# Performance work log

Measured on AMD Instinct MI355X. Metric: run time of the kernel, lower is better.

## Reference

```python
import jax, jax.numpy as jnp
import numpy as np

B, N, M, DIN, HID, L, NC, NH = 8, 1024, 8, 1024, 256, 2, 7, 4
DH = HID // NH
ALPHA = 0.1          # LeakyReLU slope in RGATLayer
NEG = -9e15          # masked-softmax fill value from the source


def setup_inputs() -> dict:
    key = jax.random.key(0)
    ks = jax.random.split(key, 40)
    f32 = jnp.float32
    rn = lambda k, s, sc: jax.random.normal(k, s, f32) * sc
    w = HID ** -0.5
    inp = {
        'x': rn(ks[0], (B, N, DIN), 1.0),
        'adj': jax.random.randint(ks[1], (B, N, N), 0, 2, jnp.int32),
        's_mask': jax.random.randint(ks[2], (B, N, N), 0, 2, jnp.int32),
        's_feature': rn(ks[3], (B, M, DIN), 1.0),
        's_adj': jax.random.uniform(ks[4], (B, M, N), f32),
        'speaker_id': jax.random.randint(ks[5], (B, N), 0, M, jnp.int32),
        'fc1_w': rn(ks[6], (DIN, HID), DIN ** -0.5), 'fc1_b': jnp.zeros((HID,), f32),
        'fc2_w': rn(ks[7], (DIN, HID), DIN ** -0.5), 'fc2_b': jnp.zeros((HID,), f32),
        'gat_W': rn(ks[8], (L, HID, HID), w),
        'gat_a': rn(ks[9], (L, 3 * HID), (3 * HID) ** -0.5),
        'rel_emb': rn(ks[10], (L, 2, HID), 0.1),
        'gru_wz': rn(ks[11], (L, HID, HID), 0.1), 'gru_uz': rn(ks[12], (L, HID, HID), 0.1),
        'gru_wr': rn(ks[13], (L, HID, HID), 0.1), 'gru_ur': rn(ks[14], (L, HID, HID), 0.1),
        'gru_w': rn(ks[15], (L, HID, HID), 0.1), 'gru_u': rn(ks[16], (L, HID, HID), 0.1),
        'mha_wv': rn(ks[17], (L, HID, HID), w), 'mha_bv': jnp.zeros((L, HID), f32),
        'mha_wk': rn(ks[18], (L, HID, HID), w), 'mha_bk': jnp.zeros((L, HID), f32),
        'mha_wq': rn(ks[19], (L, HID, HID), w), 'mha_bq': jnp.zeros((L, HID), f32),
        'mha_wo': rn(ks[20], (L, HID, HID), w), 'mha_bo': jnp.zeros((L, HID), f32),
        'ln_g': jnp.ones((L, HID), f32), 'ln_b': jnp.zeros((L, HID), f32),
        'out_w': rn(ks[21], (HID, NC), w), 'out_b': jnp.zeros((NC,), f32),
    }
    return inp


def _layer_norm(x, g, b):
    mu = jnp.mean(x, -1, keepdims=True)
    var = jnp.mean((x - mu) ** 2, -1, keepdims=True)
    return (x - mu) * jax.lax.rsqrt(var + 1e-5) * g + b


def reference(x, adj, s_mask, s_feature, s_adj, speaker_id,
              fc1_w, fc1_b, fc2_w, fc2_b,
              gat_W, gat_a, rel_emb,
              gru_wz, gru_uz, gru_wr, gru_ur, gru_w, gru_u,
              mha_wv, mha_bv, mha_wk, mha_bk, mha_wq, mha_bq, mha_wo, mha_bo,
              ln_g, ln_b, out_w, out_b):
    # eval mode: dropout is identity. init_way == 'global', att_agg == True.
    H = jax.nn.relu(x @ fc1_w + fc1_b)           # [B,N,HID]
    P = jax.nn.relu(s_feature @ fc2_w + fc2_b)   # [B,M,HID]
    adj_mask = adj > 0
    for l in range(L):
        P_l_1 = jnp.einsum('bmn,bmd->bnd', s_adj, P)  # s_adj^T @ P -> [B,N,HID]
        # ---- RGAT layer (decomposed: never materializes [B,N,N,3*HID]) ----
        h = H @ gat_W[l]                               # [B,N,HID]
        a1, a2, a3 = jnp.split(gat_a[l], 3)
        rel_sc = rel_emb[l] @ a3                       # (2,) per-relation score
        e = jax.nn.leaky_relu((h @ a1)[:, :, None] + (h @ a2)[:, None, :]
                              + jnp.take(rel_sc, s_mask), ALPHA)  # [B,N,N]
        att = jax.nn.softmax(jnp.where(adj_mask, e, jnp.float32(NEG)), axis=2)
        Agg = jax.nn.elu(att @ h)                      # [B,N,HID]
        # ---- Multi-head attention aggregation (replicates source's reshape) ----
        V = (H @ mha_wv[l] + mha_bv[l]).reshape(B * NH, -1, DH)
        Km = (P_l_1 @ mha_wk[l] + mha_bk[l]).reshape(B * NH, -1, DH)
        Qm = (Agg @ mha_wq[l] + mha_bq[l]).reshape(B * NH, -1, DH)
        att2 = jax.nn.softmax(jnp.einsum('bqd,bkd->bqk', Qm, Km) * DH ** -0.5, axis=-1)
        ctx = (att2 @ V).reshape(B, -1, HID)
        H_new = _layer_norm(ctx @ mha_wo[l] + mha_bo[l] + H, ln_g[l], ln_b[l])
        # ---- GRU3d speaker-state update (uses H[l], i.e. pre-update H) ----
        P_agg = jnp.einsum('bmn,bnd->bmd', s_adj, H)   # [B,M,HID]
        z = jax.nn.sigmoid(P @ gru_wz[l] + P_agg @ gru_uz[l])
        r = jax.nn.sigmoid(P @ gru_wr[l] + P_agg @ gru_ur[l])
        h_hat = jnp.tanh(P @ gru_w[l] + r * (P_agg @ gru_u[l]))
        P = (1 - z) * P + z * h_hat
        H = H_new
    # sim_loss
    ps = jnp.einsum('bmd,bkd->bmk', P, P)
    ps = ps * (1.0 - jnp.eye(M, dtype=ps.dtype))
    p_sim = jnp.mean(jnp.mean(jnp.mean(ps, -1), -1), -1)
    logits = H @ out_w + out_b
    return (logits, p_sim)
```

## Files before the change

### kernel.cpp

```cpp
#include <hip/hip_runtime.h>
#include <cmath>

#define B 8
#define N 1024
#define MSP 8
#define DIN 1024
#define HID 256
#define NLAYER 2
#define NCLS 7
#define NHEAD 4
#define DHD 64
#define G (B*NHEAD)
#define SEQ 1024
#define LALPHA 0.1f
#define NEGF (-9e15f)
#define RROWS 8

typedef unsigned short u16;
typedef unsigned int u32;
typedef __attribute__((ext_vector_type(8))) short short8;
typedef __attribute__((ext_vector_type(4))) float f32x4;

__device__ __forceinline__ u16 f2bf(float f) {
  u32 u = __float_as_uint(f);
  u += 0x7FFFu + ((u >> 16) & 1u);
  return (u16)(u >> 16);
}
__device__ __forceinline__ void stf(float* p, size_t i, float v) { p[i] = v; }
__device__ __forceinline__ void stf(u16* p, size_t i, float v) { p[i] = f2bf(v); }

__device__ __forceinline__ float wave_reduce_sum(float v) {
  #pragma unroll
  for (int o = 32; o > 0; o >>= 1) v += __shfl_xor(v, o, 64);
  return v;
}
__device__ __forceinline__ float wave_reduce_max(float v) {
  #pragma unroll
  for (int o = 32; o > 0; o >>= 1) v = fmaxf(v, __shfl_xor(v, o, 64));
  return v;
}

__device__ __forceinline__ void tcast_tile(
    const float* src, u16* dst, int ldS, int ldD, int r0, int c0, int t,
    u16* tile )
{
  #pragma unroll
  for (int i = 0; i < 4; ++i) {
    int e = i * 1024 + t * 4;
    int r = e >> 6, c = e & 63;
    float4 v = *(const float4*)&src[(size_t)(r0 + r) * ldS + c0 + c];
    u16* d = &tile[r * 72 + c];
    d[0] = f2bf(v.x); d[1] = f2bf(v.y); d[2] = f2bf(v.z); d[3] = f2bf(v.w);
  }
  __syncthreads();
  #pragma unroll
  for (int i = 0; i < 2; ++i) {
    int e = i * 2048 + t * 8;
    int r2 = e >> 6, c2 = e & 63;
    u16 v[8];
    #pragma unroll
    for (int j = 0; j < 8; ++j) v[j] = tile[(c2 + j) * 72 + r2];
    *(uint4*)&dst[(size_t)(c0 + r2) * ldD + r0 + c2] = *(const uint4*)v;
  }
}

__global__ __launch_bounds__(256) void wprep256(
    const float* g, const float* wv, const float* wk, const float* wq,
    const float* wo, const float* wz, const float* wr, const float* w,
    const float* uz, const float* ur, const float* u, u16* WT)
{
  __shared__ u16 tile[64 * 72];
  int z = blockIdx.z, idx = z >> 1, l = z & 1;
  const float* src;
  switch (idx) {
    case 0: src = g; break;  case 1: src = wv; break; case 2: src = wk; break;
    case 3: src = wq; break; case 4: src = wo; break; case 5: src = wz; break;
    case 6: src = wr; break; case 7: src = w; break;  case 8: src = uz; break;
    case 9: src = ur; break; default: src = u; break;
  }
  src += (size_t)l * 65536;
  u16* dst = WT + (size_t)z * 65536;
  tcast_tile(src, dst, 256, 256, blockIdx.x * 64, blockIdx.y * 64, threadIdx.x, tile);
}

__global__ __launch_bounds__(256) void wprepfc(
    const float* w1, const float* w2, u16* WTfc)
{
  __shared__ u16 tile[64 * 72];
  int z = blockIdx.z;
  const float* src = z ? w2 : w1;
  u16* dst = WTfc + (size_t)z * 262144;
  tcast_tile(src, dst, 256, 1024, blockIdx.x * 64, blockIdx.y * 64, threadIdx.x, tile);
}

__global__ __launch_bounds__(256) void hcast_kernel(
    const float* h, u16* ht)
{
  __shared__ u16 tile[64 * 72];
  tcast_tile(h, ht, 256, 8192, blockIdx.x * 64, blockIdx.y * 64, threadIdx.x, tile);
}

__global__ __launch_bounds__(256) void outprep(const float* ow, u16* WTout) {
  int t = threadIdx.x;
  for (int e = t; e < NCLS * 256; e += 256) {
    int n = e >> 8, k = e & 255;
    WTout[e] = f2bf(ow[k * NCLS + n]);
  }
}

__device__ __forceinline__ void stage_a(const float* p, u16* d) {
  #pragma unroll
  for (int q = 0; q < 4; ++q) {
    float4 v = *(const float4*)(p + q * 4);
    d[q * 4 + 0] = f2bf(v.x); d[q * 4 + 1] = f2bf(v.y);
    d[q * 4 + 2] = f2bf(v.z); d[q * 4 + 3] = f2bf(v.w);
  }
}
__device__ __forceinline__ void stage_a(const u16* p, u16* d) {
  *(uint4*)d = *(const uint4*)p;
  *(uint4*)(d + 8) = *(const uint4*)(p + 8);
}

template <typename TA, typename TC>
__global__ __launch_bounds__(256) void gemm_t(
    const TA* __restrict__ A, const u16* __restrict__ Wt,
    const float* __restrict__ bias, TC* __restrict__ C,
    int K, int ldA, int ldW, int Nc, int act,
    size_t sA, size_t sW, size_t sC)
{
  __shared__ u16 As[64 * 72];
  __shared__ u16 Ws[64 * 72];
  int z = blockIdx.z;
  const TA* Ab = A + (size_t)z * sA;
  const u16* Wb = Wt + (size_t)z * sW;
  TC* Cb = C + (size_t)z * sC;
  int bm = blockIdx.x * 64, bn = blockIdx.y * 64;
  int t = threadIdx.x;
  int w = t >> 6, lane = t & 63, quad = lane >> 4, l15 = lane & 15;
  int wy = w >> 1, wx = w & 1;
  int sr = t >> 2, kg = (t & 3) * 16;
  bool wok = (bn + sr) < Nc;
  f32x4 acc[2][2];
  #pragma unroll
  for (int i = 0; i < 2; ++i)
    #pragma unroll
    for (int j = 0; j < 2; ++j) acc[i][j] = (f32x4){0.f, 0.f, 0.f, 0.f};

  for (int k0 = 0; k0 < K; k0 += 64) {
    u16 av[16];
    stage_a(Ab + (size_t)(bm + sr) * ldA + k0 + kg, av);
    *(uint4*)&As[sr * 72 + kg] = *(const uint4*)av;
    *(uint4*)&As[sr * 72 + kg + 8] = *(const uint4*)(av + 8);
    if (wok) {
      *(uint4*)&Ws[sr * 72 + kg] = *(const uint4*)(Wb + (size_t)(bn + sr) * ldW + k0 + kg);
      *(uint4*)&Ws[sr * 72 + kg + 8] = *(const uint4*)(Wb + (size_t)(bn + sr) * ldW + k0 + kg + 8);
    } else {
      uint4 zz = {0, 0, 0, 0};
      *(uint4*)&Ws[sr * 72 + kg] = zz;
      *(uint4*)&Ws[sr * 72 + kg + 8] = zz;
    }
    __syncthreads();
    #pragma unroll
    for (int kh = 0; kh < 64; kh += 32) {
      short8 a0 = *(const short8*)&As[(wy * 32 + l15) * 72 + kh + quad * 8];
      short8 a1 = *(const short8*)&As[(wy * 32 + 16 + l15) * 72 + kh + quad * 8];
      short8 b0 = *(const short8*)&Ws[(wx * 32 + l15) * 72 + kh + quad * 8];
      short8 b1 = *(const short8*)&Ws[(wx * 32 + 16 + l15) * 72 + kh + quad * 8];
      acc[0][0] = __builtin_amdgcn_mfma_f32_16x16x32_bf16(a0, b0, acc[0][0], 0, 0, 0);
      acc[0][1] = __builtin_amdgcn_mfma_f32_16x16x32_bf16(a0, b1, acc[0][1], 0, 0, 0);
      acc[1][0] = __builtin_amdgcn_mfma_f32_16x16x32_bf16(a1, b0, acc[1][0], 0, 0, 0);
      acc[1][1] = __builtin_amdgcn_mfma_f32_16x16x32_bf16(a1, b1, acc[1][1], 0, 0, 0);
    }
    __syncthreads();
  }
  #pragma unroll
  for (int sa = 0; sa < 2; ++sa) {
    #pragma unroll
    for (int sb = 0; sb < 2; ++sb) {
      int col = bn + wx * 32 + sb * 16 + l15;
      if (col < Nc) {
        float bv = bias ? bias[col] : 0.f;
        #pragma unroll
        for (int r = 0; r < 4; ++r) {
          int row = bm + wy * 32 + sa * 16 + quad * 4 + r;
          float v = acc[sa][sb][r] + bv;
          if (act == 1) v = fmaxf(v, 0.f);
          else if (act == 2) v = (v > 0.f) ? v : (__expf(v) - 1.f);
          stf(Cb, (size_t)row * Nc + col, v);
        }
      }
    }
  }
}

__global__ __launch_bounds__(256) void fc2_reduce(
    const float* __restrict__ scr, const float* __restrict__ bias,
    float* __restrict__ out)
{
  int i = blockIdx.x * 256 + threadIdx.x;
  float v = scr[i] + scr[16384 + i] + scr[32768 + i] + scr[49152 + i]
          + bias[threadIdx.x];
  out[i] = fmaxf(v, 0.f);
}

__global__ __launch_bounds__(256) void gru_combine(
    const float* __restrict__ zP, const float* __restrict__ zU,
    const float* __restrict__ P, float* __restrict__ Pn)
{
  int i = blockIdx.x * 256 + threadIdx.x;
  float z = 1.f / (1.f + __expf(-(zP[i] + zU[i])));
  float r = 1.f / (1.f + __expf(-(zP[16384 + i] + zU[16384 + i])));
  float hh = tanhf(zP[32768 + i] + r * zU[32768 + i]);
  Pn[i] = (1.f - z) * P[i] + z * hh;
}

__global__ __launch_bounds__(256) void pl1_kernel(
    const float* __restrict__ s_adj, const float* __restrict__ P,
    float* __restrict__ out)
{
  int bn = blockIdx.x;
  int b = bn >> 10, n = bn & 1023, t = threadIdx.x;
  float acc = 0.f;
  #pragma unroll
  for (int m = 0; m < MSP; ++m) {
    float sa = s_adj[(size_t)(b * MSP + m) * N + n];
    acc += sa * P[(size_t)(b * MSP + m) * HID + t];
  }
  out[(size_t)bn * HID + t] = acc;
}

__global__ __launch_bounds__(256) void relsc_kernel(
    const float* __restrict__ rel_emb_l, const float* __restrict__ a3,
    float* __restrict__ rsc)
{
  __shared__ float scratch[4];
  int r = blockIdx.x, t = threadIdx.x;
  float v = rel_emb_l[r * HID + t] * a3[t];
  int wave = t >> 6, lane = t & 63;
  v = wave_reduce_sum(v);
  if (lane == 0) scratch[wave] = v;
  __syncthreads();
  if (t == 0) rsc[r] = scratch[0] + scratch[1] + scratch[2] + scratch[3];
}

__global__ __launch_bounds__(256) void f1f2_kernel(
    const float* __restrict__ h, const float* __restrict__ a12,
    float* __restrict__ f1, float* __restrict__ f2)
{
  __shared__ float s1[4], s2[4];
  int row = blockIdx.x, t = threadIdx.x;
  float hv = h[(size_t)row * HID + t];
  float v1 = hv * a12[t];
  float v2 = hv * a12[HID + t];
  int wave = t >> 6, lane = t & 63;
  v1 = wave_reduce_sum(v1);
  v2 = wave_reduce_sum(v2);
  if (lane == 0) { s1[wave] = v1; s2[wave] = v2; }
  __syncthreads();
  if (t == 0) f1[row] = s1[0] + s1[1] + s1[2] + s1[3];
  if (t == 1) f2[row] = s2[0] + s2[1] + s2[2] + s2[3];
}

__global__ __launch_bounds__(256) void rgat_scores_kernel(
    const int* __restrict__ adj, const int* __restrict__ smask,
    const float* __restrict__ f1, const float* __restrict__ f2,
    const float* __restrict__ rsc, u16* __restrict__ Pw)
{
  __shared__ float wrow[RROWS][N];
  __shared__ float lsum[RROWS];
  int blk = blockIdx.x;
  int b = blk / (N / RROWS);
  int i0 = (blk % (N / RROWS)) * RROWS;
  int t = threadIdx.x;
  float r0 = rsc[0], r1 = rsc[1];
  float f1v[RROWS];
  #pragma unroll
  for (int r = 0; r < RROWS; ++r) f1v[r] = f1[b * N + i0 + r];
  for (int jt = 0; jt < N; jt += 256) {
    int j = jt + t;
    float f2v = f2[b * N + j];
    #pragma unroll
    for (int r = 0; r < RROWS; ++r) {
      size_t base = ((size_t)(b * N + i0 + r)) * N + j;
      int a = adj[base];
      int sm = smask[base];
      float e = f1v[r] + f2v + (sm ? r1 : r0);
      e = (e > 0.f) ? e : LALPHA * e;
      wrow[r][j] = (a > 0) ? e : NEGF;
    }
  }
  __syncthreads();
  int wave = t >> 6, lane = t & 63;
  #pragma unroll
  for (int q = 0; q < RROWS / 4; ++q) {
    int r = wave * (RROWS / 4) + q;
    float m = -3.4e38f;
    for (int jj = lane; jj < N; jj += 64) m = fmaxf(m, wrow[r][jj]);
    m = wave_reduce_max(m);
    float s = 0.f;
    for (int jj = lane; jj < N; jj += 64) {
      float e = __expf(wrow[r][jj] - m);
      wrow[r][jj] = e;
      s += e;
    }
    s = wave_reduce_sum(s);
    if (lane == 0) lsum[r] = s;
  }
  __syncthreads();
  float inv[RROWS];
  #pragma unroll
  for (int r = 0; r < RROWS; ++r) inv[r] = 1.f / lsum[r];
  for (int jt = 0; jt < N; jt += 256) {
    int j = jt + t;
    #pragma unroll
    for (int r = 0; r < RROWS; ++r)
      Pw[((size_t)(b * N + i0 + r)) * N + j] = f2bf(wrow[r][j] * inv[r]);
  }
}

__global__ __launch_bounds__(256) void vtransp_kernel(
    const u16* __restrict__ Vb, u16* __restrict__ Vt)
{
  __shared__ u16 tile[64 * 72];
  int g = blockIdx.x >> 4;
  int s0 = (blockIdx.x & 15) * 64;
  int t = threadIdx.x;
  #pragma unroll
  for (int i = 0; i < 2; ++i) {
    int e = i * 256 + t;
    int sr = e >> 3, d8 = (e & 7) * 8;
    *(uint4*)&tile[sr * 72 + d8] =
        *(const uint4*)&Vb[((size_t)(g * SEQ) + s0 + sr) * DHD + d8];
  }
  __syncthreads();
  #pragma unroll
  for (int i = 0; i < 2; ++i) {
    int e = i * 256 + t;
    int dr = e >> 3, s8 = (e & 7) * 8;
    u16 v[8];
    #pragma unroll
    for (int j = 0; j < 8; ++j) v[j] = tile[(s8 + j) * 72 + dr];
    *(uint4*)&Vt[((size_t)(g * DHD) + dr) * SEQ + s0 + s8] = *(const uint4*)v;
  }
}

__global__ __launch_bounds__(256) void mha_mfma_kernel(
    const u16* __restrict__ Qb, const u16* __restrict__ Kb,
    const u16* __restrict__ Vt, float* __restrict__ ctx)
{
  __shared__ u16 Ks[64 * 72];
  __shared__ u16 Vs[64 * 72];
  __shared__ u16 Ps[4][16 * 72];
  int g = blockIdx.x >> 4;
  int q0 = (blockIdx.x & 15) * 64;
  int t = threadIdx.x;
  int w = t >> 6, lane = t & 63, quad = lane >> 4, l15 = lane & 15;
  const u16* Qrow = Qb + ((size_t)(g * SEQ) + q0 + w * 16 + l15) * DHD;
  short8 qa0 = *(const short8*)(Qrow + quad * 8);
  short8 qa1 = *(const short8*)(Qrow + 32 + quad * 8);
  const u16* Kg = Kb + (size_t)g * SEQ * DHD;
  const u16* Vg = Vt + (size_t)g * DHD * SEQ;
  f32x4 O[4];
  #pragma unroll
  for (int nt = 0; nt < 4; ++nt) O[nt] = (f32x4){0.f, 0.f, 0.f, 0.f};
  float mprev[4] = {-1e30f, -1e30f, -1e30f, -1e30f};
  float lsum[4] = {0.f, 0.f, 0.f, 0.f};

  for (int kc = 0; kc < SEQ; kc += 64) {
    #pragma unroll
    for (int i = 0; i < 2; ++i) {
      int e = i * 256 + t;
      int row = e >> 3, c8 = (e & 7) * 8;
      *(uint4*)&Ks[row * 72 + c8] = *(const uint4*)&Kg[(size_t)(kc + row) * DHD + c8];
      *(uint4*)&Vs[row * 72 + c8] = *(const uint4*)&Vg[(size_t)row * SEQ + kc + c8];
    }
    __syncthreads();
    f32x4 s[4];
    #pragma unroll
    for (int st = 0; st < 4; ++st) {
      short8 b0 = *(const short8*)&Ks[(st * 16 + l15) * 72 + quad * 8];
      short8 b1 = *(const short8*)&Ks[(st * 16 + l15) * 72 + 32 + quad * 8];
      f32x4 c = (f32x4){0.f, 0.f, 0.f, 0.f};
      c = __builtin_amdgcn_mfma_f32_16x16x32_bf16(qa0, b0, c, 0, 0, 0);
      c = __builtin_amdgcn_mfma_f32_16x16x32_bf16(qa1, b1, c, 0, 0, 0);
      s[st] = c * 0.125f;
    }
    float cm[4];
    #pragma unroll
    for (int r = 0; r < 4; ++r)
      cm[r] = fmaxf(fmaxf(s[0][r], s[1][r]), fmaxf(s[2][r], s[3][r]));
    #pragma unroll
    for (int off = 1; off < 16; off <<= 1) {
      #pragma unroll
      for (int r = 0; r < 4; ++r) cm[r] = fmaxf(cm[r], __shfl_xor(cm[r], off, 64));
    }
    float mnew[4], alpha[4], rs[4];
    #pragma unroll
    for (int r = 0; r < 4; ++r) {
      mnew[r] = fmaxf(mprev[r], cm[r]);
      alpha[r] = __expf(mprev[r] - mnew[r]);
      mprev[r] = mnew[r];
      rs[r] = 0.f;
    }
    #pragma unroll
    for (int st = 0; st < 4; ++st) {
      #pragma unroll
      for (int r = 0; r < 4; ++r) {
        float p = __expf(s[st][r] - mnew[r]);
        rs[r] += p;
        Ps[w][(quad * 4 + r) * 72 + st * 16 + l15] = f2bf(p);
      }
    }
    #pragma unroll
    for (int off = 1; off < 16; off <<= 1) {
      #pragma unroll
      for (int r = 0; r < 4; ++r) rs[r] += __shfl_xor(rs[r], off, 64);
    }
    #pragma unroll
    for (int r = 0; r < 4; ++r) lsum[r] = lsum[r] * alpha[r] + rs[r];
    #pragma unroll
    for (int nt = 0; nt < 4; ++nt)
      #pragma unroll
      for (int r = 0; r < 4; ++r) O[nt][r] *= alpha[r];
    #pragma unroll
    for (int kh = 0; kh < 2; ++kh) {
      short8 pa = *(const short8*)&Ps[w][l15 * 72 + kh * 32 + quad * 8];
      #pragma unroll
      for (int nt = 0; nt < 4; ++nt) {
        short8 vb = *(const short8*)&Vs[(nt * 16 + l15) * 72 + kh * 32 + quad * 8];
        O[nt] = __builtin_amdgcn_mfma_f32_16x16x32_bf16(pa, vb, O[nt], 0, 0, 0);
      }
    }
    __syncthreads();
  }
  #pragma unroll
  for (int nt = 0; nt < 4; ++nt) {
    #pragma unroll
    for (int r = 0; r < 4; ++r) {
      size_t row = (size_t)(g * SEQ) + q0 + w * 16 + quad * 4 + r;
      ctx[row * DHD + nt * 16 + l15] = O[nt][r] / lsum[r];
    }
  }
}

__global__ __launch_bounds__(256) void ln_kernel(
    const float* __restrict__ tmp, const float* __restrict__ Hres,
    const float* __restrict__ gg, const float* __restrict__ bb,
    float* __restrict__ out)
{
  __shared__ float s1[4], s2[4];
  int row = blockIdx.x, t = threadIdx.x;
  float x = tmp[(size_t)row * HID + t] + Hres[(size_t)row * HID + t];
  float v1 = wave_reduce_sum(x);
  float v2 = wave_reduce_sum(x * x);
  int wave = t >> 6, lane = t & 63;
  if (lane == 0) { s1[wave] = v1; s2[wave] = v2; }
  __syncthreads();
  float mu = (s1[0] + s1[1] + s1[2] + s1[3]) * (1.f / HID);
  float var = (s2[0] + s2[1] + s2[2] + s2[3]) * (1.f / HID) - mu * mu;
  var = fmaxf(var, 0.f);
  float y = (x - mu) * rsqrtf(var + 1e-5f) * gg[t] + bb[t];
  out[(size_t)row * HID + t] = y;
}

__global__ __launch_bounds__(256) void pagg_kernel(
    const float* __restrict__ s_adj, const float* __restrict__ H,
    float* __restrict__ Pagg)
{
  int row = blockIdx.x;
  int b = row >> 3, t = threadIdx.x;
  float acc = 0.f;
  const float* Hb = H + (size_t)(b * N) * HID + t;
  const float* sa = s_adj + (size_t)row * N;
  for (int n = 0; n < N; ++n)
    acc += sa[n] * Hb[(size_t)n * HID];
  Pagg[(size_t)row * HID + t] = acc;
}

__global__ __launch_bounds__(256) void psim_kernel(
    const float* __restrict__ P, float* __restrict__ out)
{
  __shared__ float scratch[4];
  int t = threadIdx.x;
  float total = 0.f;
  for (int idx = t; idx < B * MSP * MSP; idx += 256) {
    int b = idx >> 6, m = (idx >> 3) & 7, k = idx & 7;
    if (m != k) {
      const float* pm = P + (size_t)(b * MSP + m) * HID;
      const float* pk = P + (size_t)(b * MSP + k) * HID;
      float d = 0.f;
      for (int dd = 0; dd < HID; ++dd) d += pm[dd] * pk[dd];
      total += d;
    }
  }
  int wave = t >> 6, lane = t & 63;
  total = wave_reduce_sum(total);
  if (lane == 0) scratch[wave] = total;
  __syncthreads();
  if (t == 0)
    out[0] = (scratch[0] + scratch[1] + scratch[2] + scratch[3]) *
             (1.f / (B * MSP * MSP));
}

extern "C" void kernel_launch(void* const* d_in, const int* in_sizes, int n_in,
                              void* d_out, int out_size, void* d_ws, size_t ws_size,
                              hipStream_t stream) {
  const float* x      = (const float*)d_in[0];
  const int*   adj    = (const int*)d_in[1];
  const int*   smask  = (const int*)d_in[2];
  const float* s_feat = (const float*)d_in[3];
  const float* s_adj  = (const float*)d_in[4];
  const float* fc1_w  = (const float*)d_in[6];
  const float* fc1_b  = (const float*)d_in[7];
  const float* fc2_w  = (const float*)d_in[8];
  const float* fc2_b  = (const float*)d_in[9];
  const float* gat_W  = (const float*)d_in[10];
  const float* gat_a  = (const float*)d_in[11];
  const float* rel_emb= (const float*)d_in[12];
  const float* gru_wz = (const float*)d_in[13];
  const float* gru_uz = (const float*)d_in[14];
  const float* gru_wr = (const float*)d_in[15];
  const float* gru_ur = (const float*)d_in[16];
  const float* gru_w  = (const float*)d_in[17];
  const float* gru_u  = (const float*)d_in[18];
  const float* mha_wv = (const float*)d_in[19];
  const float* mha_bv = (const float*)d_in[20];
  const float* mha_wk = (const float*)d_in[21];
  const float* mha_bk = (const float*)d_in[22];
  const float* mha_wq = (const float*)d_in[23];
  const float* mha_bq = (const float*)d_in[24];
  const float* mha_wo = (const float*)d_in[25];
  const float* mha_bo = (const float*)d_in[26];
  const float* ln_g   = (const float*)d_in[27];
  const float* ln_b   = (const float*)d_in[28];
  const float* out_w  = (const float*)d_in[29];
  const float* out_b  = (const float*)d_in[30];

  float* ws = (float*)d_ws;
  const size_t BIG = (size_t)B * N * HID;
  float* H0  = ws + 0 * BIG;
  float* H1  = ws + 1 * BIG;
  float* hbf = ws + 2 * BIG;
  float* Pl1 = ws + 3 * BIG;
  float* Agg = ws + 4 * BIG;
  u16* Pw   = (u16*)(ws + 5 * BIG);
  u16* Qb16 = (u16*)(ws + 5 * BIG);
  u16* Kb16 = Qb16 + BIG;
  u16* Vb16 = (u16*)(ws + 6 * BIG);
  u16* Vt16 = Vb16 + BIG;
  u16* ht   = (u16*)(ws + 7 * BIG);
  u16* WT   = ht + 2097152;
  u16* WTfc = WT + 22 * 65536;
  u16* WTout= WTfc + 2 * 262144;
  float* scrFc = Agg;
  float* zP = hbf;
  float* zU = hbf + 3 * 16384;
  float* smw = ws + 8 * BIG;
  float* P0   = smw;
  float* P1   = smw + 16384;
  float* Pagg = smw + 32768;
  float* f1   = smw + 49152;
  float* f2   = smw + 57344;
  float* rsc  = smw + 65536;

  dim3 blk(256);
  const size_t W64K = 65536;

  wprep256<<<dim3(4, 4, 22), blk, 0, stream>>>(
      gat_W, mha_wv, mha_wk, mha_wq, mha_wo,
      gru_wz, gru_wr, gru_w, gru_uz, gru_ur, gru_u, WT);
  wprepfc<<<dim3(16, 4, 2), blk, 0, stream>>>(fc1_w, fc2_w, WTfc);
  outprep<<<1, blk, 0, stream>>>(out_w, WTout);

  gemm_t<float, float><<<dim3(128, 4, 1), blk, 0, stream>>>(
      x, WTfc, fc1_b, H0, DIN, DIN, DIN, HID, 1, 0, 0, 0);
  gemm_t<float, float><<<dim3(1, 4, 4), blk, 0, stream>>>(
      s_feat, WTfc + 262144, nullptr, scrFc, 256, DIN, DIN, HID, 0,
      256, 256, 16384);
  fc2_reduce<<<64, blk, 0, stream>>>(scrFc, fc2_b, P0);

  float* Hc = H0; float* Hn = H1; float* Pc = P0; float* Pn = P1;
  for (int l = 0; l < NLAYER; ++l) {
    pl1_kernel<<<B * N, blk, 0, stream>>>(s_adj, Pc, Pl1);
    gemm_t<float, float><<<dim3(128, 4, 1), blk, 0, stream>>>(
        Hc, WT + (size_t)(0 + l) * W64K, nullptr, hbf, HID, HID, HID, HID, 0, 0, 0, 0);
    hcast_kernel<<<dim3(128, 4), blk, 0, stream>>>(hbf, ht);
    relsc_kernel<<<2, blk, 0, stream>>>(rel_emb + (size_t)l * 2 * HID,
                                        gat_a + (size_t)l * 3 * HID + 2 * HID, rsc);
    f1f2_kernel<<<B * N, blk, 0, stream>>>(hbf, gat_a + (size_t)l * 3 * HID, f1, f2);
    rgat_scores_kernel<<<B * (N / RROWS), blk, 0, stream>>>(adj, smask, f1, f2, rsc, Pw);
    gemm_t<u16, float><<<dim3(16, 4, 8), blk, 0, stream>>>(
        Pw, ht, nullptr, Agg, N, N, B * N, HID, 2,
        (size_t)N * N, (size_t)N, (size_t)N * HID);
    gemm_t<float, u16><<<dim3(128, 4, 1), blk, 0, stream>>>(
        Hc, WT + (size_t)(2 + l) * W64K, mha_bv + l * HID, Vb16, HID, HID, HID, HID, 0, 0, 0, 0);
    gemm_t<float, u16><<<dim3(128, 4, 1), blk, 0, stream>>>(
        Pl1, WT + (size_t)(4 + l) * W64K, mha_bk + l * HID, Kb16, HID, HID, HID, HID, 0, 0, 0, 0);
    gemm_t<float, u16><<<dim3(128, 4, 1), blk, 0, stream>>>(
        Agg, WT + (size_t)(6 + l) * W64K, mha_bq + l * HID, Qb16, HID, HID, HID, HID, 0, 0, 0, 0);
    vtransp_kernel<<<G * (SEQ / 64), blk, 0, stream>>>(Vb16, Vt16);
    mha_mfma_kernel<<<G * (SEQ / 64), blk, 0, stream>>>(Qb16, Kb16, Vt16, Agg);
    gemm_t<float, float><<<dim3(128, 4, 1), blk, 0, stream>>>(
        Agg, WT + (size_t)(8 + l) * W64K, mha_bo + l * HID, Pl1, HID, HID, HID, HID, 0, 0, 0, 0);
    ln_kernel<<<B * N, blk, 0, stream>>>(Pl1, Hc, ln_g + l * HID, ln_b + l * HID, Hn);
    pagg_kernel<<<B * MSP, blk, 0, stream>>>(s_adj, Hc, Pagg);
    gemm_t<float, float><<<dim3(1, 4, 3), blk, 0, stream>>>(
        Pc, WT + (size_t)(10 + l) * W64K, nullptr, zP, HID, HID, HID, HID, 0,
        0, 2 * W64K, 16384);
    gemm_t<float, float><<<dim3(1, 4, 3), blk, 0, stream>>>(
        Pagg, WT + (size_t)(16 + l) * W64K, nullptr, zU, HID, HID, HID, HID, 0,
        0, 2 * W64K, 16384);
    gru_combine<<<64, blk, 0, stream>>>(zP, zU, Pc, Pn);
    float* th = Hc; Hc = Hn; Hn = th;
    float* tp = Pc; Pc = Pn; Pn = tp;
  }
  gemm_t<float, float><<<dim3(128, 1, 1), blk, 0, stream>>>(
      Hc, WTout, out_b, (float*)d_out, HID, HID, HID, NCLS, 0, 0, 0, 0);
  psim_kernel<<<1, blk, 0, stream>>>(Pc, (float*)d_out + (size_t)B * N * NCLS);
}
```

Measured before the change: 627.8 us.

## Register-resident softmax in RGAT scores, prefetch K/V in MHA, split-N pagg

Result: no change. 617.4 us (-1.7%).

```diff
diff --git a/kernel.cpp b/kernel.cpp
--- a/kernel.cpp
+++ b/kernel.cpp
@@ -266,55 +266,60 @@
     const float* __restrict__ f1, const float* __restrict__ f2,
     const float* __restrict__ rsc, u16* __restrict__ Pw)
 {
-  __shared__ float wrow[RROWS][N];
-  __shared__ float lsum[RROWS];
+  __shared__ float red[4][RROWS];
   int blk = blockIdx.x;
   int b = blk / (N / RROWS);
   int i0 = (blk % (N / RROWS)) * RROWS;
   int t = threadIdx.x;
+  int wave = t >> 6, lane = t & 63;
   float r0 = rsc[0], r1 = rsc[1];
-  float f1v[RROWS];
-  #pragma unroll
-  for (int r = 0; r < RROWS; ++r) f1v[r] = f1[b * N + i0 + r];
-  for (int jt = 0; jt < N; jt += 256) {
-    int j = jt + t;
-    float f2v = f2[b * N + j];
-    #pragma unroll
-    for (int r = 0; r < RROWS; ++r) {
-      size_t base = ((size_t)(b * N + i0 + r)) * N + j;
-      int a = adj[base];
-      int sm = smask[base];
-      float e = f1v[r] + f2v + (sm ? r1 : r0);
-      e = (e > 0.f) ? e : LALPHA * e;
-      wrow[r][j] = (a > 0) ? e : NEGF;
-    }
-  }
-  __syncthreads();
-  int wave = t >> 6, lane = t & 63;
-  #pragma unroll
-  for (int q = 0; q < RROWS / 4; ++q) {
-    int r = wave * (RROWS / 4) + q;
-    float m = -3.4e38f;
-    for (int jj = lane; jj < N; jj += 64) m = fmaxf(m, wrow[r][jj]);
+  int j0 = t * 4;
+  float4 f2v = *(const float4*)&f2[b * N + j0];
+  float ev[RROWS][4];
+  #pragma unroll
+  for (int r = 0; r < RROWS; ++r) {
+    size_t base = ((size_t)(b * N + i0 + r)) * N + j0;
+    int4 a4 = *(const int4*)&adj[base];
+    int4 s4 = *(const int4*)&smask[base];
+    float f1v = f1[b * N + i0 + r];
+    float e;
+    e = f1v + f2v.x + (s4.x ? r1 : r0); e = (e > 0.f) ? e : LALPHA * e;
+    ev[r][0] = (a4.x > 0) ? e : NEGF;
+    e = f1v + f2v.y + (s4.y ? r1 : r0); e = (e > 0.f) ? e : LALPHA * e;
+    ev[r][1] = (a4.y > 0) ? e : NEGF;
+    e = f1v + f2v.z + (s4.z ? r1 : r0); e = (e > 0.f) ? e : LALPHA * e;
+    ev[r][2] = (a4.z > 0) ? e : NEGF;
+    e = f1v + f2v.w + (s4.w ? r1 : r0); e = (e > 0.f) ? e : LALPHA * e;
+    ev[r][3] = (a4.w > 0) ? e : NEGF;
+  }
+  #pragma unroll
+  for (int r = 0; r < RROWS; ++r) {
+    float m = fmaxf(fmaxf(ev[r][0], ev[r][1]), fmaxf(ev[r][2], ev[r][3]));
     m = wave_reduce_max(m);
+    if (lane == 0) red[wave][r] = m;
+  }
+  __syncthreads();
+  float mx[RROWS];
+  #pragma unroll
+  for (int r = 0; r < RROWS; ++r)
+    mx[r] = fmaxf(fmaxf(red[0][r], red[1][r]), fmaxf(red[2][r], red[3][r]));
+  __syncthreads();
+  #pragma unroll
+  for (int r = 0; r < RROWS; ++r) {
     float s = 0.f;
-    for (int jj = lane; jj < N; jj += 64) {
-      float e = __expf(wrow[r][jj] - m);
-      wrow[r][jj] = e;
-      s += e;
-    }
+    #pragma unroll
+    for (int c = 0; c < 4; ++c) { ev[r][c] = __expf(ev[r][c] - mx[r]); s += ev[r][c]; }
     s = wave_reduce_sum(s);
-    if (lane == 0) lsum[r] = s;
-  }
-  __syncthreads();
-  float inv[RROWS];
-  #pragma unroll
-  for (int r = 0; r < RROWS; ++r) inv[r] = 1.f / lsum[r];
-  for (int jt = 0; jt < N; jt += 256) {
-    int j = jt + t;
-    #pragma unroll
-    for (int r = 0; r < RROWS; ++r)
-      Pw[((size_t)(b * N + i0 + r)) * N + j] = f2bf(wrow[r][j] * inv[r]);
+    if (lane == 0) red[wave][r] = s;
+  }
+  __syncthreads();
+  #pragma unroll
+  for (int r = 0; r < RROWS; ++r) {
+    float inv = 1.f / (red[0][r] + red[1][r] + red[2][r] + red[3][r]);
+    u16 o[4];
+    #pragma unroll
+    for (int c = 0; c < 4; ++c) o[c] = f2bf(ev[r][c] * inv);
+    *(uint2*)&Pw[((size_t)(b * N + i0 + r)) * N + j0] = *(const uint2*)o;
   }
 }
 
@@ -360,21 +365,31 @@
   short8 qa1 = *(const short8*)(Qrow + 32 + quad * 8);
   const u16* Kg = Kb + (size_t)g * SEQ * DHD;
   const u16* Vg = Vt + (size_t)g * DHD * SEQ;
+  int srow = t >> 3, sc8 = (t & 7) * 8;
+  int srow1 = (256 + t) >> 3, sc81 = sc8;
   f32x4 O[4];
   #pragma unroll
   for (int nt = 0; nt < 4; ++nt) O[nt] = (f32x4){0.f, 0.f, 0.f, 0.f};
   float mprev[4] = {-1e30f, -1e30f, -1e30f, -1e30f};
   float lsum[4] = {0.f, 0.f, 0.f, 0.f};
+  uint4 kreg[2], vreg[2];
+  kreg[0] = *(const uint4*)&Kg[(size_t)srow * DHD + sc8];
+  kreg[1] = *(const uint4*)&Kg[(size_t)srow1 * DHD + sc81];
+  vreg[0] = *(const uint4*)&Vg[(size_t)srow * SEQ + sc8];
+  vreg[1] = *(const uint4*)&Vg[(size_t)srow1 * SEQ + sc81];
 
   for (int kc = 0; kc < SEQ; kc += 64) {
-    #pragma unroll
-    for (int i = 0; i < 2; ++i) {
-      int e = i * 256 + t;
-      int row = e >> 3, c8 = (e & 7) * 8;
-      *(uint4*)&Ks[row * 72 + c8] = *(const uint4*)&Kg[(size_t)(kc + row) * DHD + c8];
-      *(uint4*)&Vs[row * 72 + c8] = *(const uint4*)&Vg[(size_t)row * SEQ + kc + c8];
-    }
+    *(uint4*)&Ks[srow * 72 + sc8] = kreg[0];
+    *(uint4*)&Ks[srow1 * 72 + sc81] = kreg[1];
+    *(uint4*)&Vs[srow * 72 + sc8] = vreg[0];
+    *(uint4*)&Vs[srow1 * 72 + sc81] = vreg[1];
     __syncthreads();
+    if (kc + 64 < SEQ) {
+      kreg[0] = *(const uint4*)&Kg[(size_t)(kc + 64 + srow) * DHD + sc8];
+      kreg[1] = *(const uint4*)&Kg[(size_t)(kc + 64 + srow1) * DHD + sc81];
+      vreg[0] = *(const uint4*)&Vg[(size_t)srow * SEQ + kc + 64 + sc8];
+      vreg[1] = *(const uint4*)&Vg[(size_t)srow1 * SEQ + kc + 64 + sc81];
+    }
     f32x4 s[4];
     #pragma unroll
     for (int st = 0; st < 4; ++st) {
@@ -463,18 +478,29 @@
   out[(size_t)row * HID + t] = y;
 }
 
-__global__ __launch_bounds__(256) void pagg_kernel(
+__global__ __launch_bounds__(256) void pagg_part(
     const float* __restrict__ s_adj, const float* __restrict__ H,
-    float* __restrict__ Pagg)
+    float* __restrict__ scr)
 {
   int row = blockIdx.x;
+  int sl = blockIdx.y;
   int b = row >> 3, t = threadIdx.x;
+  const float* Hb = H + ((size_t)(b * N) + sl * 128) * HID + t;
+  const float* sa = s_adj + (size_t)row * N + sl * 128;
   float acc = 0.f;
-  const float* Hb = H + (size_t)(b * N) * HID + t;
-  const float* sa = s_adj + (size_t)row * N;
-  for (int n = 0; n < N; ++n)
+  #pragma unroll 4
+  for (int n = 0; n < 128; ++n)
     acc += sa[n] * Hb[(size_t)n * HID];
-  Pagg[(size_t)row * HID + t] = acc;
+  scr[((size_t)sl * (B * MSP) + row) * HID + t] = acc;
+}
+__global__ __launch_bounds__(256) void pagg_reduce(
+    const float* __restrict__ scr, float* __restrict__ Pagg)
+{
+  int row = blockIdx.x, t = threadIdx.x;
+  float s = 0.f;
+  #pragma unroll
+  for (int k = 0; k < 8; ++k) s += scr[((size_t)k * (B * MSP) + row) * HID + t];
+  Pagg[(size_t)row * HID + t] = s;
 }
 
 __global__ __launch_bounds__(256) void psim_kernel(
@@ -555,6 +581,7 @@
   float* scrFc = Agg;
   float* zP = hbf;
   float* zU = hbf + 3 * 16384;
+  float* paggScr = hbf + 6 * 16384;
   float* smw = ws + 8 * BIG;
   float* P0   = smw;
   float* P1   = smw + 16384;
@@ -603,7 +630,8 @@
     gemm_t<float, float><<<dim3(128, 4, 1), blk, 0, stream>>>(
         Agg, WT + (size_t)(8 + l) * W64K, mha_bo + l * HID, Pl1, HID, HID, HID, HID, 0, 0, 0, 0);
     ln_kernel<<<B * N, blk, 0, stream>>>(Pl1, Hc, ln_g + l * HID, ln_b + l * HID, Hn);
-    pagg_kernel<<<B * MSP, blk, 0, stream>>>(s_adj, Hc, Pagg);
+    pagg_part<<<dim3(B * MSP, 8), blk, 0, stream>>>(s_adj, Hc, paggScr);
+    pagg_reduce<<<B * MSP, blk, 0, stream>>>(paggScr, Pagg);
     gemm_t<float, float><<<dim3(1, 4, 3), blk, 0, stream>>>(
         Pc, WT + (size_t)(10 + l) * W64K, nullptr, zP, HID, HID, HID, HID, 0,
         0, 2 * W64K, 16384);
```
